# Kernel tuning notes

Measured on AMD Instinct MI355X. Metric: run time of the kernel, lower is better.

The kernel has to match this reference:

```python
import jax, jax.numpy as jnp
import numpy as np

VOCAB = 5000
HID = 256
BATCH = 64
STEPS = 256


def setup_inputs() -> dict:
    key = jax.random.key(0)
    ks = jax.random.split(key, 7)
    scale_k = 1.0 / np.sqrt(VOCAB)
    scale_r = 1.0 / np.sqrt(HID)
    return {
        "tokens": jax.random.randint(ks[0], (BATCH, STEPS), 0, VOCAB, dtype=jnp.int32),
        "h0": jnp.zeros((BATCH, HID), dtype=jnp.float32),
        # GRUCell params (Keras reset_after=True layout): kernel [V,3H], recurrent [H,3H], bias [2,3H]
        "kernel": jax.random.normal(ks[1], (VOCAB, 3 * HID), dtype=jnp.float32) * scale_k,
        "rkernel": jax.random.normal(ks[2], (HID, 3 * HID), dtype=jnp.float32) * scale_r,
        "bias": jnp.zeros((2, 3 * HID), dtype=jnp.float32),
        # final Dense(vocab_size)
        "Wd": jax.random.normal(ks[3], (HID, VOCAB), dtype=jnp.float32) * scale_r,
        "bd": jnp.zeros((VOCAB,), dtype=jnp.float32),
    }


def reference(tokens, h0, kernel, rkernel, bias, Wd, bd):
    # X = one_hot(transpose(inputs), vocab)  -> time-major [T, B, V]
    X = jax.nn.one_hot(tokens.T, VOCAB, dtype=kernel.dtype)

    b_in, b_rec = bias[0], bias[1]

    def step(h, x):  # x: [B, V], h: [B, H]
        mx = x @ kernel + b_in            # [B, 3H]
        mh = h @ rkernel + b_rec          # [B, 3H]
        xz, xr, xh = jnp.split(mx, 3, axis=-1)
        hz, hr, hh = jnp.split(mh, 3, axis=-1)
        z = jax.nn.sigmoid(xz + hz)
        r = jax.nn.sigmoid(xr + hr)
        cand = jnp.tanh(xh + r * hh)      # reset_after=True candidate
        h_new = z * h + (1.0 - z) * cand
        return h_new, h_new

    h_last, Y = jax.lax.scan(step, h0, X)  # Y: [T, B, H]
    out = Y.reshape(-1, Y.shape[-1]) @ Wd + bd  # [T*B, V]
    return out, h_last
```

## Files before the change

kernel.cpp:

```cpp
#include <hip/hip_runtime.h>
#include <cstdint>

typedef __attribute__((ext_vector_type(8))) short bf16x8;
typedef __attribute__((ext_vector_type(4))) float f32x4;
typedef unsigned short u16;
typedef unsigned int u32;
typedef unsigned long long u64;

#define T_STEPS 256
#define BATCH 64
#define HID 256
#define VOCAB 5000
#define KC 768
#define NWG 16
#define HB 16
#define NPAD 5120

__device__ __forceinline__ u16 f2bf(float x) {
  union { float f; u32 u; } v; v.f = x;
  u32 r = v.u + 0x7fffu + ((v.u >> 16) & 1u);
  return (u16)(r >> 16);
}
__device__ __forceinline__ float bf2f(u16 b) {
  union { float f; u32 u; } v; v.u = ((u32)b) << 16;
  return v.f;
}
__device__ __forceinline__ void load_lds16(const void* g, void* l) {
  __builtin_amdgcn_global_load_lds(
      (const __attribute__((address_space(1))) void*)g,
      (__attribute__((address_space(3))) void*)l, 16, 0, 0);
}
__device__ __forceinline__ void st_u16_coh(u16* p, u16 v) {
  asm volatile("global_store_short %0, %1, off sc0 sc1" :: "v"(p), "v"((u32)v));
}
__device__ __forceinline__ u64 ld_u64_coh(const u16* p) {
  return __hip_atomic_load((const u64*)p, __ATOMIC_RELAXED, __HIP_MEMORY_SCOPE_AGENT);
}
__device__ __forceinline__ float fsig(float x) {
  return __builtin_amdgcn_rcpf(1.f + __expf(-x));
}
__device__ __forceinline__ float ftanh(float x) {
  return 1.f - 2.f * __builtin_amdgcn_rcpf(1.f + __expf(2.f * x));
}

__global__ __launch_bounds__(256) void prep_b(const float* __restrict__ Wd,
                                              u16* __restrict__ BT) {
  int gid = blockIdx.x * 256 + threadIdx.x;
  int n = gid / 96;
  int k0 = (gid % 96) * 8;
  union { uint4 q; u16 s[8]; } o;
#pragma unroll
  for (int i = 0; i < 8; ++i) {
    int k = k0 + i;
    float x = 0.f;
    if (n < VOCAB) {
      int kk = (k < 512) ? (k & 255) : (k - 512);
      x = Wd[kk * VOCAB + n];
    }
    u16 hi = f2bf(x);
    o.s[i] = (k < 512) ? hi : f2bf(x - bf2f(hi));
  }
  *(uint4*)(BT + (size_t)n * KC + k0) = o.q;
}

__global__ __launch_bounds__(256) void prep_h0(const float* __restrict__ h0,
                                               u16* __restrict__ H0S) {
  int i = blockIdx.x * 256 + threadIdx.x;
  int b = i >> 8, j = i & 255;
  float x = h0[i];
  u16 hi = f2bf(x);
  u16 lo = f2bf(x - bf2f(hi));
  H0S[b * KC + j] = hi;
  H0S[b * KC + 256 + j] = lo;
}

__global__ __launch_bounds__(256, 1) void gru_rec(
    const int* __restrict__ tokens, const float* __restrict__ h0,
    const float* __restrict__ ker, const float* __restrict__ rker,
    const float* __restrict__ bias,
    u16* __restrict__ Abuf, const u16* __restrict__ H0S,
    float* __restrict__ hlast, u32* __restrict__ flags) {
  const int g = blockIdx.x;
  const int tid = threadIdx.x;
  const int w = tid >> 6;
  const int l = tid & 63;
  const int lm = l & 15;
  const int lq = l >> 4;

  int cmap[3]; float brec[3], bin[3];
#pragma unroll
  for (int nt = 0; nt < 3; ++nt) {
    cmap[nt] = nt * 256 + g * HB + lm;
    bin[nt]  = bias[cmap[nt]];
    brec[nt] = bias[KC + cmap[nt]];
  }

  bf16x8 Bhi[3][8], Blo[3][8];
#pragma unroll
  for (int nt = 0; nt < 3; ++nt)
#pragma unroll
    for (int kb = 0; kb < 8; ++kb) {
      union { bf16x8 v; u16 s[8]; } uh, ul;
#pragma unroll
      for (int jj = 0; jj < 8; ++jj) {
        int k = kb * 32 + lq * 8 + jj;
        float x = rker[k * KC + cmap[nt]];
        u16 hi = f2bf(x);
        uh.s[jj] = hi;
        ul.s[jj] = f2bf(x - bf2f(hi));
      }
      Bhi[nt][kb] = uh.v; Blo[nt][kb] = ul.v;
    }

  float hown[4];
#pragma unroll
  for (int r = 0; r < 4; ++r)
    hown[r] = h0[(16 * w + lq * 4 + r) * HID + g * HB + lm];

  const int rowloc = 16 * w + lm;

  int ntok[4];
#pragma unroll
  for (int r = 0; r < 4; ++r)
    ntok[r] = tokens[(16 * w + lq * 4 + r) * T_STEPS];

  for (int t = 0; t < T_STEPS; ++t) {
    int ctok[4];
#pragma unroll
    for (int r = 0; r < 4; ++r) ctok[r] = ntok[r];
    if (t + 1 < T_STEPS) {
#pragma unroll
      for (int r = 0; r < 4; ++r)
        ntok[r] = tokens[(16 * w + lq * 4 + r) * T_STEPS + t + 1];
    }

    float mx[3][4];
#pragma unroll
    for (int r = 0; r < 4; ++r) {
#pragma unroll
      for (int nt = 0; nt < 3; ++nt)
        mx[nt][r] = ker[(size_t)ctok[r] * KC + cmap[nt]] + bin[nt];
    }

    if (t > 0) {
      const u32 tt = (u32)t;
      int guard = 0;
      for (;;) {
        u32 v = __hip_atomic_load(&flags[l * 32], __ATOMIC_RELAXED,
                                  __HIP_MEMORY_SCOPE_AGENT);
        if (__all((int)(v >= tt))) break;
        if (++guard > (1 << 24)) break;
        __builtin_amdgcn_s_sleep(1);
      }
    }

    const u16* hsrc = (t == 0) ? H0S : (Abuf + (size_t)(t - 1) * BATCH * KC);
    const u16* hrow = hsrc + (size_t)rowloc * KC;
    bf16x8 Ahi[8], Alo[8];
#pragma unroll
    for (int kb = 0; kb < 8; ++kb) {
      union { u64 d[2]; bf16x8 v; } a0, a1;
      const u16* p0 = hrow + kb * 32 + lq * 8;
      const u16* p1 = hrow + 256 + kb * 32 + lq * 8;
      a0.d[0] = ld_u64_coh(p0);
      a0.d[1] = ld_u64_coh(p0 + 4);
      a1.d[0] = ld_u64_coh(p1);
      a1.d[1] = ld_u64_coh(p1 + 4);
      Ahi[kb] = a0.v; Alo[kb] = a1.v;
    }

    f32x4 acc[3];
#pragma unroll
    for (int nt = 0; nt < 3; ++nt)
      acc[nt] = (f32x4){brec[nt], brec[nt], brec[nt], brec[nt]};

#pragma unroll
    for (int kb = 0; kb < 8; ++kb) {
#pragma unroll
      for (int nt = 0; nt < 3; ++nt) {
        acc[nt] = __builtin_amdgcn_mfma_f32_16x16x32_bf16(Ahi[kb], Bhi[nt][kb], acc[nt], 0, 0, 0);
        acc[nt] = __builtin_amdgcn_mfma_f32_16x16x32_bf16(Alo[kb], Bhi[nt][kb], acc[nt], 0, 0, 0);
        acc[nt] = __builtin_amdgcn_mfma_f32_16x16x32_bf16(Ahi[kb], Blo[nt][kb], acc[nt], 0, 0, 0);
      }
    }

#pragma unroll
    for (int r = 0; r < 4; ++r) {
      float z  = fsig(acc[0][r] + mx[0][r]);
      float rr = fsig(acc[1][r] + mx[1][r]);
      float cd = ftanh(mx[2][r] + rr * acc[2][r]);
      float hn = z * hown[r] + (1.f - z) * cd;
      hown[r] = hn;
      u16 hi = f2bf(hn);
      u16 lo = f2bf(hn - bf2f(hi));
      int b = 16 * w + lq * 4 + r;
      u16* orow = Abuf + (size_t)(t * BATCH + b) * KC;
      st_u16_coh(orow + g * HB + lm, hi);
      st_u16_coh(orow + 256 + g * HB + lm, lo);
      orow[512 + g * HB + lm] = hi;
    }

    asm volatile("s_waitcnt vmcnt(0)" ::: "memory");
    if (l == 0)
      __hip_atomic_store(&flags[(g * 4 + w) * 32], (u32)(t + 1), __ATOMIC_RELAXED,
                         __HIP_MEMORY_SCOPE_AGENT);
    asm volatile("" ::: "memory");
  }

#pragma unroll
  for (int r = 0; r < 4; ++r) {
    int b = 16 * w + lq * 4 + r;
    hlast[b * HID + g * HB + lm] = hown[r];
  }
}

__global__ __launch_bounds__(256, 2) void gemm_out(
    const u16* __restrict__ A, const u16* __restrict__ BT,
    const float* __restrict__ bd, float* __restrict__ out) {
  __shared__ u16 As[128 * 32];
  __shared__ u16 Bs[128 * 32];
  const int tid = threadIdx.x;
  const int w = tid >> 6, l = tid & 63;
  const int lm = l & 15, lq = l >> 4;
  const int wm = w & 1, wn = w >> 1;
  const int m0 = blockIdx.y * 128;
  const int n0 = blockIdx.x * 128;
  const int tr = tid >> 2;
  const int tc = (tid & 3) * 8;

  f32x4 acc[4][4] = {};

  for (int kb = 0; kb < 24; ++kb) {
    if (kb) __syncthreads();
#pragma unroll
    for (int j = 0; j < 2; ++j) {
      load_lds16(A  + (size_t)(m0 + j * 64 + tr) * KC + kb * 32 + tc,
                 As + j * 2048 + (tid >> 6) * 512);
      load_lds16(BT + (size_t)(n0 + j * 64 + tr) * KC + kb * 32 + tc,
                 Bs + j * 2048 + (tid >> 6) * 512);
    }
    __syncthreads();

    bf16x8 af[4], bfr[4];
#pragma unroll
    for (int mi = 0; mi < 4; ++mi)
      af[mi] = *(const bf16x8*)(As + (wm * 64 + mi * 16 + lm) * 32 + lq * 8);
#pragma unroll
    for (int ni = 0; ni < 4; ++ni)
      bfr[ni] = *(const bf16x8*)(Bs + (wn * 64 + ni * 16 + lm) * 32 + lq * 8);
#pragma unroll
    for (int mi = 0; mi < 4; ++mi)
#pragma unroll
      for (int ni = 0; ni < 4; ++ni)
        acc[mi][ni] = __builtin_amdgcn_mfma_f32_16x16x32_bf16(af[mi], bfr[ni], acc[mi][ni], 0, 0, 0);
  }

#pragma unroll
  for (int ni = 0; ni < 4; ++ni) {
    int n = n0 + wn * 64 + ni * 16 + lm;
    float bdv = (n < VOCAB) ? bd[n] : 0.f;
#pragma unroll
    for (int mi = 0; mi < 4; ++mi) {
#pragma unroll
      for (int r = 0; r < 4; ++r) {
        int m = m0 + wm * 64 + mi * 16 + lq * 4 + r;
        if (n < VOCAB) out[(size_t)m * VOCAB + n] = acc[mi][ni][r] + bdv;
      }
    }
  }
}

extern "C" void kernel_launch(void* const* d_in, const int* in_sizes, int n_in,
                              void* d_out, int out_size, void* d_ws, size_t ws_size,
                              hipStream_t stream) {
  const int*   tokens = (const int*)d_in[0];
  const float* h0     = (const float*)d_in[1];
  const float* ker    = (const float*)d_in[2];
  const float* rker   = (const float*)d_in[3];
  const float* bias   = (const float*)d_in[4];
  const float* Wd     = (const float*)d_in[5];
  const float* bd     = (const float*)d_in[6];
  float* out = (float*)d_out;
  char* ws = (char*)d_ws;

  u16* Abuf  = (u16*)(ws);
  u16* BT    = (u16*)(ws + 25165824);
  u16* H0S   = (u16*)(ws + 33030144);
  u32* flags = (u32*)(ws + 33128448);

  hipMemsetAsync(flags, 0, 8192, stream);
  prep_b<<<1920, 256, 0, stream>>>(Wd, BT);
  prep_h0<<<64, 256, 0, stream>>>(h0, H0S);
  gru_rec<<<NWG, 256, 0, stream>>>(tokens, h0, ker, rker, bias, Abuf, H0S,
                                   out + (size_t)16384 * VOCAB, flags);
  gemm_out<<<dim3(40, 128), 256, 0, stream>>>(Abuf, BT, bd, out);
}
```

Baseline: 2.254 ms.

## Fuse GRU recurrence and output GEMM into one persistent kernel with flag-gated tiles

```diff
diff --git a/kernel.cpp b/kernel.cpp
--- a/kernel.cpp
+++ b/kernel.cpp
@@ -15,6 +15,7 @@
 #define NWG 16
 #define HB 16
 #define NPAD 5120
+#define NTILES 5120
 
 __device__ __forceinline__ u16 f2bf(float x) {
   union { float f; u32 u; } v; v.f = x;
@@ -74,197 +75,227 @@
   H0S[b * KC + 256 + j] = lo;
 }
 
-__global__ __launch_bounds__(256, 1) void gru_rec(
+__global__ __launch_bounds__(256, 1) void fused(
     const int* __restrict__ tokens, const float* __restrict__ h0,
     const float* __restrict__ ker, const float* __restrict__ rker,
     const float* __restrict__ bias,
-    u16* __restrict__ Abuf, const u16* __restrict__ H0S,
-    float* __restrict__ hlast, u32* __restrict__ flags) {
-  const int g = blockIdx.x;
-  const int tid = threadIdx.x;
-  const int w = tid >> 6;
-  const int l = tid & 63;
-  const int lm = l & 15;
-  const int lq = l >> 4;
-
-  int cmap[3]; float brec[3], bin[3];
-#pragma unroll
-  for (int nt = 0; nt < 3; ++nt) {
-    cmap[nt] = nt * 256 + g * HB + lm;
-    bin[nt]  = bias[cmap[nt]];
-    brec[nt] = bias[KC + cmap[nt]];
-  }
-
-  bf16x8 Bhi[3][8], Blo[3][8];
-#pragma unroll
-  for (int nt = 0; nt < 3; ++nt)
-#pragma unroll
-    for (int kb = 0; kb < 8; ++kb) {
-      union { bf16x8 v; u16 s[8]; } uh, ul;
-#pragma unroll
-      for (int jj = 0; jj < 8; ++jj) {
-        int k = kb * 32 + lq * 8 + jj;
-        float x = rker[k * KC + cmap[nt]];
-        u16 hi = f2bf(x);
-        uh.s[jj] = hi;
-        ul.s[jj] = f2bf(x - bf2f(hi));
-      }
-      Bhi[nt][kb] = uh.v; Blo[nt][kb] = ul.v;
-    }
-
-  float hown[4];
-#pragma unroll
-  for (int r = 0; r < 4; ++r)
-    hown[r] = h0[(16 * w + lq * 4 + r) * HID + g * HB + lm];
-
-  const int rowloc = 16 * w + lm;
-
-  int ntok[4];
-#pragma unroll
-  for (int r = 0; r < 4; ++r)
-    ntok[r] = tokens[(16 * w + lq * 4 + r) * T_STEPS];
-
-  for (int t = 0; t < T_STEPS; ++t) {
-    int ctok[4];
-#pragma unroll
-    for (int r = 0; r < 4; ++r) ctok[r] = ntok[r];
-    if (t + 1 < T_STEPS) {
-#pragma unroll
-      for (int r = 0; r < 4; ++r)
-        ntok[r] = tokens[(16 * w + lq * 4 + r) * T_STEPS + t + 1];
-    }
-
-    float mx[3][4];
-#pragma unroll
-    for (int r = 0; r < 4; ++r) {
-#pragma unroll
-      for (int nt = 0; nt < 3; ++nt)
-        mx[nt][r] = ker[(size_t)ctok[r] * KC + cmap[nt]] + bin[nt];
-    }
-
-    if (t > 0) {
-      const u32 tt = (u32)t;
-      int guard = 0;
-      for (;;) {
-        u32 v = __hip_atomic_load(&flags[l * 32], __ATOMIC_RELAXED,
-                                  __HIP_MEMORY_SCOPE_AGENT);
-        if (__all((int)(v >= tt))) break;
-        if (++guard > (1 << 24)) break;
-        __builtin_amdgcn_s_sleep(1);
-      }
-    }
-
-    const u16* hsrc = (t == 0) ? H0S : (Abuf + (size_t)(t - 1) * BATCH * KC);
-    const u16* hrow = hsrc + (size_t)rowloc * KC;
-    bf16x8 Ahi[8], Alo[8];
-#pragma unroll
-    for (int kb = 0; kb < 8; ++kb) {
-      union { u64 d[2]; bf16x8 v; } a0, a1;
-      const u16* p0 = hrow + kb * 32 + lq * 8;
-      const u16* p1 = hrow + 256 + kb * 32 + lq * 8;
-      a0.d[0] = ld_u64_coh(p0);
-      a0.d[1] = ld_u64_coh(p0 + 4);
-      a1.d[0] = ld_u64_coh(p1);
-      a1.d[1] = ld_u64_coh(p1 + 4);
-      Ahi[kb] = a0.v; Alo[kb] = a1.v;
-    }
-
-    f32x4 acc[3];
-#pragma unroll
-    for (int nt = 0; nt < 3; ++nt)
-      acc[nt] = (f32x4){brec[nt], brec[nt], brec[nt], brec[nt]};
-
-#pragma unroll
-    for (int kb = 0; kb < 8; ++kb) {
-#pragma unroll
-      for (int nt = 0; nt < 3; ++nt) {
-        acc[nt] = __builtin_amdgcn_mfma_f32_16x16x32_bf16(Ahi[kb], Bhi[nt][kb], acc[nt], 0, 0, 0);
-        acc[nt] = __builtin_amdgcn_mfma_f32_16x16x32_bf16(Alo[kb], Bhi[nt][kb], acc[nt], 0, 0, 0);
-        acc[nt] = __builtin_amdgcn_mfma_f32_16x16x32_bf16(Ahi[kb], Blo[nt][kb], acc[nt], 0, 0, 0);
-      }
-    }
-
-#pragma unroll
-    for (int r = 0; r < 4; ++r) {
-      float z  = fsig(acc[0][r] + mx[0][r]);
-      float rr = fsig(acc[1][r] + mx[1][r]);
-      float cd = ftanh(mx[2][r] + rr * acc[2][r]);
-      float hn = z * hown[r] + (1.f - z) * cd;
-      hown[r] = hn;
-      u16 hi = f2bf(hn);
-      u16 lo = f2bf(hn - bf2f(hi));
-      int b = 16 * w + lq * 4 + r;
-      u16* orow = Abuf + (size_t)(t * BATCH + b) * KC;
-      st_u16_coh(orow + g * HB + lm, hi);
-      st_u16_coh(orow + 256 + g * HB + lm, lo);
-      orow[512 + g * HB + lm] = hi;
-    }
-
-    asm volatile("s_waitcnt vmcnt(0)" ::: "memory");
-    if (l == 0)
-      __hip_atomic_store(&flags[(g * 4 + w) * 32], (u32)(t + 1), __ATOMIC_RELAXED,
-                         __HIP_MEMORY_SCOPE_AGENT);
-    asm volatile("" ::: "memory");
-  }
-
-#pragma unroll
-  for (int r = 0; r < 4; ++r) {
-    int b = 16 * w + lq * 4 + r;
-    hlast[b * HID + g * HB + lm] = hown[r];
-  }
-}
-
-__global__ __launch_bounds__(256, 2) void gemm_out(
-    const u16* __restrict__ A, const u16* __restrict__ BT,
-    const float* __restrict__ bd, float* __restrict__ out) {
+    u16* Abuf, const u16* __restrict__ H0S,
+    float* __restrict__ hlast, u32* flags,
+    const u16* __restrict__ BT, const float* __restrict__ bd,
+    float* __restrict__ out) {
   __shared__ u16 As[128 * 32];
   __shared__ u16 Bs[128 * 32];
+  __shared__ u32 stile;
+
   const int tid = threadIdx.x;
+
+  if (blockIdx.x < NWG) {
+    const int g = blockIdx.x;
+    const int w = tid >> 6;
+    const int l = tid & 63;
+    const int lm = l & 15;
+    const int lq = l >> 4;
+
+    int cmap[3]; float brec[3], bin[3];
+#pragma unroll
+    for (int nt = 0; nt < 3; ++nt) {
+      cmap[nt] = nt * 256 + g * HB + lm;
+      bin[nt]  = bias[cmap[nt]];
+      brec[nt] = bias[KC + cmap[nt]];
+    }
+
+    bf16x8 Bhi[3][8], Blo[3][8];
+#pragma unroll
+    for (int nt = 0; nt < 3; ++nt)
+#pragma unroll
+      for (int kb = 0; kb < 8; ++kb) {
+        union { bf16x8 v; u16 s[8]; } uh, ul;
+#pragma unroll
+        for (int jj = 0; jj < 8; ++jj) {
+          int k = kb * 32 + lq * 8 + jj;
+          float x = rker[k * KC + cmap[nt]];
+          u16 hi = f2bf(x);
+          uh.s[jj] = hi;
+          ul.s[jj] = f2bf(x - bf2f(hi));
+        }
+        Bhi[nt][kb] = uh.v; Blo[nt][kb] = ul.v;
+      }
+
+    float hown[4];
+#pragma unroll
+    for (int r = 0; r < 4; ++r)
+      hown[r] = h0[(16 * w + lq * 4 + r) * HID + g * HB + lm];
+
+    const int rowloc = 16 * w + lm;
+
+    int ntok[4];
+#pragma unroll
+    for (int r = 0; r < 4; ++r)
+      ntok[r] = tokens[(16 * w + lq * 4 + r) * T_STEPS];
+
+    for (int t = 0; t < T_STEPS; ++t) {
+      int ctok[4];
+#pragma unroll
+      for (int r = 0; r < 4; ++r) ctok[r] = ntok[r];
+      if (t + 1 < T_STEPS) {
+#pragma unroll
+        for (int r = 0; r < 4; ++r)
+          ntok[r] = tokens[(16 * w + lq * 4 + r) * T_STEPS + t + 1];
+      }
+
+      float mx[3][4];
+#pragma unroll
+      for (int r = 0; r < 4; ++r) {
+#pragma unroll
+        for (int nt = 0; nt < 3; ++nt)
+          mx[nt][r] = ker[(size_t)ctok[r] * KC + cmap[nt]] + bin[nt];
+      }
+
+      if (t > 0) {
+        const u32 tt = (u32)t;
+        int guard = 0;
+        for (;;) {
+          u32 v = __hip_atomic_load(&flags[l * 32], __ATOMIC_RELAXED,
+                                    __HIP_MEMORY_SCOPE_AGENT);
+          if (__all((int)(v >= tt))) break;
+          if (++guard > (1 << 24)) break;
+          __builtin_amdgcn_s_sleep(1);
+        }
+      }
+
+      const u16* hsrc = (t == 0) ? H0S : (Abuf + (size_t)(t - 1) * BATCH * KC);
+      const u16* hrow = hsrc + (size_t)rowloc * KC;
+      bf16x8 Ahi[8], Alo[8];
+#pragma unroll
+      for (int kb = 0; kb < 8; ++kb) {
+        union { u64 d[2]; bf16x8 v; } a0, a1;
+        const u16* p0 = hrow + kb * 32 + lq * 8;
+        const u16* p1 = hrow + 256 + kb * 32 + lq * 8;
+        a0.d[0] = ld_u64_coh(p0);
+        a0.d[1] = ld_u64_coh(p0 + 4);
+        a1.d[0] = ld_u64_coh(p1);
+        a1.d[1] = ld_u64_coh(p1 + 4);
+        Ahi[kb] = a0.v; Alo[kb] = a1.v;
+      }
+
+      f32x4 acc[3];
+#pragma unroll
+      for (int nt = 0; nt < 3; ++nt)
+        acc[nt] = (f32x4){brec[nt], brec[nt], brec[nt], brec[nt]};
+
+#pragma unroll
+      for (int kb = 0; kb < 8; ++kb) {
+#pragma unroll
+        for (int nt = 0; nt < 3; ++nt) {
+          acc[nt] = __builtin_amdgcn_mfma_f32_16x16x32_bf16(Ahi[kb], Bhi[nt][kb], acc[nt], 0, 0, 0);
+          acc[nt] = __builtin_amdgcn_mfma_f32_16x16x32_bf16(Alo[kb], Bhi[nt][kb], acc[nt], 0, 0, 0);
+          acc[nt] = __builtin_amdgcn_mfma_f32_16x16x32_bf16(Ahi[kb], Blo[nt][kb], acc[nt], 0, 0, 0);
+        }
+      }
+
+#pragma unroll
+      for (int r = 0; r < 4; ++r) {
+        float z  = fsig(acc[0][r] + mx[0][r]);
+        float rr = fsig(acc[1][r] + mx[1][r]);
+        float cd = ftanh(mx[2][r] + rr * acc[2][r]);
+        float hn = z * hown[r] + (1.f - z) * cd;
+        hown[r] = hn;
+        u16 hi = f2bf(hn);
+        u16 lo = f2bf(hn - bf2f(hi));
+        int b = 16 * w + lq * 4 + r;
+        u16* orow = Abuf + (size_t)(t * BATCH + b) * KC;
+        st_u16_coh(orow + g * HB + lm, hi);
+        st_u16_coh(orow + 256 + g * HB + lm, lo);
+        st_u16_coh(orow + 512 + g * HB + lm, hi);
+      }
+
+      asm volatile("s_waitcnt vmcnt(0)" ::: "memory");
+      if (l == 0)
+        __hip_atomic_store(&flags[(g * 4 + w) * 32], (u32)(t + 1), __ATOMIC_RELAXED,
+                           __HIP_MEMORY_SCOPE_AGENT);
+      asm volatile("" ::: "memory");
+    }
+
+#pragma unroll
+    for (int r = 0; r < 4; ++r) {
+      int b = 16 * w + lq * 4 + r;
+      hlast[b * HID + g * HB + lm] = hown[r];
+    }
+    return;
+  }
+
+  u32* counter = flags + 16;
   const int w = tid >> 6, l = tid & 63;
   const int lm = l & 15, lq = l >> 4;
   const int wm = w & 1, wn = w >> 1;
-  const int m0 = blockIdx.y * 128;
-  const int n0 = blockIdx.x * 128;
-  const int tr = tid >> 2;
-  const int tc = (tid & 3) * 8;
-
-  f32x4 acc[4][4] = {};
-
-  for (int kb = 0; kb < 24; ++kb) {
-    if (kb) __syncthreads();
-#pragma unroll
-    for (int j = 0; j < 2; ++j) {
-      load_lds16(A  + (size_t)(m0 + j * 64 + tr) * KC + kb * 32 + tc,
-                 As + j * 2048 + (tid >> 6) * 512);
-      load_lds16(BT + (size_t)(n0 + j * 64 + tr) * KC + kb * 32 + tc,
-                 Bs + j * 2048 + (tid >> 6) * 512);
-    }
+
+  for (;;) {
     __syncthreads();
-
-    bf16x8 af[4], bfr[4];
-#pragma unroll
-    for (int mi = 0; mi < 4; ++mi)
-      af[mi] = *(const bf16x8*)(As + (wm * 64 + mi * 16 + lm) * 32 + lq * 8);
-#pragma unroll
-    for (int ni = 0; ni < 4; ++ni)
-      bfr[ni] = *(const bf16x8*)(Bs + (wn * 64 + ni * 16 + lm) * 32 + lq * 8);
-#pragma unroll
-    for (int mi = 0; mi < 4; ++mi)
-#pragma unroll
-      for (int ni = 0; ni < 4; ++ni)
-        acc[mi][ni] = __builtin_amdgcn_mfma_f32_16x16x32_bf16(af[mi], bfr[ni], acc[mi][ni], 0, 0, 0);
-  }
-
-#pragma unroll
-  for (int ni = 0; ni < 4; ++ni) {
-    int n = n0 + wn * 64 + ni * 16 + lm;
-    float bdv = (n < VOCAB) ? bd[n] : 0.f;
-#pragma unroll
-    for (int mi = 0; mi < 4; ++mi) {
-#pragma unroll
-      for (int r = 0; r < 4; ++r) {
-        int m = m0 + wm * 64 + mi * 16 + lq * 4 + r;
-        if (n < VOCAB) out[(size_t)m * VOCAB + n] = acc[mi][ni][r] + bdv;
+    if (tid == 0)
+      stile = __hip_atomic_fetch_add(counter, 1u, __ATOMIC_RELAXED,
+                                     __HIP_MEMORY_SCOPE_AGENT);
+    __syncthreads();
+    const u32 tile = stile;
+    if (tile >= NTILES) break;
+    const int mi = (int)(tile / 40);
+    const int ni = (int)(tile % 40);
+    const int m0 = mi * 128;
+    const int n0 = ni * 128;
+
+    if (tid < 64) {
+      const u32 need = (u32)(2 * mi + 2);
+      int guard = 0;
+      for (;;) {
+        u32 v = __hip_atomic_load(&flags[tid * 32], __ATOMIC_RELAXED,
+                                  __HIP_MEMORY_SCOPE_AGENT);
+        if (__all((int)(v >= need))) break;
+        if (++guard > (1 << 22)) break;
+        __builtin_amdgcn_s_sleep(16);
+      }
+    }
+    __syncthreads();
+
+    const int tr = tid >> 2;
+    const int tc = (tid & 3) * 8;
+
+    f32x4 acc[4][4] = {};
+
+    for (int kb = 0; kb < 24; ++kb) {
+      if (kb) __syncthreads();
+#pragma unroll
+      for (int j = 0; j < 2; ++j) {
+        load_lds16(Abuf + (size_t)(m0 + j * 64 + tr) * KC + kb * 32 + tc,
+                   As + j * 2048 + w * 512);
+        load_lds16(BT   + (size_t)(n0 + j * 64 + tr) * KC + kb * 32 + tc,
+                   Bs + j * 2048 + w * 512);
+      }
+      __syncthreads();
+
+      bf16x8 af[4], bfr[4];
+#pragma unroll
+      for (int mi2 = 0; mi2 < 4; ++mi2)
+        af[mi2] = *(const bf16x8*)(As + (wm * 64 + mi2 * 16 + lm) * 32 + lq * 8);
+#pragma unroll
+      for (int ni2 = 0; ni2 < 4; ++ni2)
+        bfr[ni2] = *(const bf16x8*)(Bs + (wn * 64 + ni2 * 16 + lm) * 32 + lq * 8);
+#pragma unroll
+      for (int mi2 = 0; mi2 < 4; ++mi2)
+#pragma unroll
+        for (int ni2 = 0; ni2 < 4; ++ni2)
+          acc[mi2][ni2] = __builtin_amdgcn_mfma_f32_16x16x32_bf16(af[mi2], bfr[ni2], acc[mi2][ni2], 0, 0, 0);
+    }
+
+#pragma unroll
+    for (int ni2 = 0; ni2 < 4; ++ni2) {
+      int n = n0 + wn * 64 + ni2 * 16 + lm;
+      float bdv = (n < VOCAB) ? bd[n] : 0.f;
+#pragma unroll
+      for (int mi2 = 0; mi2 < 4; ++mi2) {
+#pragma unroll
+        for (int r = 0; r < 4; ++r) {
+          int m = m0 + wm * 64 + mi2 * 16 + lq * 4 + r;
+          if (n < VOCAB) out[(size_t)m * VOCAB + n] = acc[mi2][ni2][r] + bdv;
+        }
       }
     }
   }
@@ -291,7 +322,7 @@
   hipMemsetAsync(flags, 0, 8192, stream);
   prep_b<<<1920, 256, 0, stream>>>(Wd, BT);
   prep_h0<<<64, 256, 0, stream>>>(h0, H0S);
-  gru_rec<<<NWG, 256, 0, stream>>>(tokens, h0, ker, rker, bias, Abuf, H0S,
-                                   out + (size_t)16384 * VOCAB, flags);
-  gemm_out<<<dim3(40, 128), 256, 0, stream>>>(Abuf, BT, bd, out);
-}
+  fused<<<256, 256, 0, stream>>>(tokens, h0, ker, rker, bias, Abuf, H0S,
+                                 out + (size_t)16384 * VOCAB, flags,
+                                 BT, bd, out);
+}
```

After: 2.264 ms. Within noise of the previous version (+0.4%).
